# Kernel tuning notes

Hardware: AMD Instinct MI355X
Metric: run time of the kernel (lower is better)

The kernel has to match this reference:

```python
import jax, jax.numpy as jnp
import numpy as np

EPS = 1e-6
NMS_THR = 0.5
PULL_W = 1.0
PUSH_W = 1.0


def bbox_overlaps(a, b):
    # a: [M,4], b: [N,4] in (x1,y1,x2,y2) -> IoU [M,N]
    area_a = (a[:, 2] - a[:, 0]) * (a[:, 3] - a[:, 1])
    area_b = (b[:, 2] - b[:, 0]) * (b[:, 3] - b[:, 1])
    lt = jnp.maximum(a[:, None, :2], b[None, :, :2])
    rb = jnp.minimum(a[:, None, 2:], b[None, :, 2:])
    wh = jnp.clip(rb - lt, 0.0)
    inter = wh[..., 0] * wh[..., 1]
    return inter / (area_a[:, None] + area_b[None, :] - inter + EPS)


def _single_nms_loss(gti, gt_box, proposals):
    # gti: [N] int, gt_box: [G,4], proposals: [N,5]
    N = proposals.shape[0]
    G = gt_box.shape[0]
    boxes = proposals[:, :4]
    scores = proposals[:, 4]
    # push_select=True: first arg of proposal-proposal IoU is detached
    iou = bbox_overlaps(jax.lax.stop_gradient(boxes), boxes)      # [N,N]
    gpi = bbox_overlaps(gt_box, boxes)                            # [G,N]
    gpi_per = gpi[gti, jnp.arange(N)]                             # gt_proposal_iou[gt_inds[s], s]
    sg_scores = jax.lax.stop_gradient(scores)

    pos = gti >= 0
    n_pos = jnp.sum(pos)
    zero = jnp.zeros((), proposals.dtype)
    rec0 = jnp.full((G,), -1, jnp.int32)   # max_score_box_rec: gt -> box idx

    def step(carry, _):
        active, rec, pull_sum, push_sum, pull_cnt, push_cnt = carry
        any_act = jnp.any(active)
        i = jnp.argmax(jnp.where(active, scores, -jnp.inf))
        i_gt = gti[i]
        rem = active.at[i].set(False)
        has_rem = jnp.any(rem)
        body_valid = any_act & has_rem  # torch breaks before adding losses if idx empty

        # ----- pull -----
        seen = rec[i_gt] >= 0
        max_idx = jnp.maximum(rec[i_gt], 0)
        max_s_iou = jnp.maximum(iou[max_idx, i], EPS)
        pull = -jnp.log(1.0 - NMS_THR + max_s_iou) * sg_scores[i]
        pull_sum = pull_sum + jnp.where(any_act & seen & has_rem, pull, 0.0)
        pull_cnt = pull_cnt + jnp.where(any_act & seen, 1.0, 0.0)  # incremented before break
        new_val = jnp.where(any_act & ~seen, i.astype(rec.dtype), rec[i_gt])
        rec = rec.at[i_gt].set(new_val)

        # ----- push -----
        overlap = rem & (iou[i] > NMS_THR)
        push_mask = overlap & (gti != i_gt)
        has_push = jnp.any(push_mask)
        seen_s = rec[gti] >= 0  # rec already contains i_gt here (matches torch order)
        q = push_mask & (~seen_s)
        cnt = jnp.sum(q.astype(scores.dtype)) + EPS
        per = -jnp.log(EPS + gpi_per) * sg_scores
        push = jnp.sum(jnp.where(q, per, 0.0)) / cnt
        push_sum = push_sum + jnp.where(body_valid & has_push, push, 0.0)
        push_cnt = push_cnt + jnp.where(body_valid & has_push, 1.0, 0.0)

        active_next = rem & (~overlap)
        return (active_next, rec, pull_sum, push_sum, pull_cnt, push_cnt), None

    init = (pos, rec0, zero, zero, zero, zero)
    (_, _, pull_sum, push_sum, pull_cnt, push_cnt), _ = jax.lax.scan(step, init, None, length=N)

    gate = (n_pos > 1).astype(proposals.dtype)  # early-return when <=1 positive
    pull = gate * pull_sum / (pull_cnt + EPS)
    push = gate * push_sum / (push_cnt + EPS)
    return push, pull


def setup_inputs() -> dict:
    key = jax.random.key(0)
    k0, k1, k2, k3, k4, k5, k6 = jax.random.split(key, 7)
    B, N, G = 8, 2048, 64
    anchor_gt_inds = jax.random.randint(k0, (B, N), 0, G)
    # valid GT boxes: centers in a 1000x1000 image, sizes in [16,128]
    cx = jax.random.uniform(k1, (B, G)) * 1000.0
    cy = jax.random.uniform(k2, (B, G)) * 1000.0
    w = 16.0 + jax.random.uniform(k3, (B, G)) * 112.0
    h = 16.0 + jax.random.uniform(k4, (B, G)) * 112.0
    gt_bboxes = jnp.stack([cx - w / 2, cy - h / 2, cx + w / 2, cy + h / 2], axis=-1).astype(jnp.float32)
    # proposals jitter around their assigned GT so pull/push branches trigger
    pb = gt_bboxes[jnp.arange(B)[:, None], anchor_gt_inds] + jax.random.normal(k5, (B, N, 4)) * 6.0
    x1 = jnp.minimum(pb[..., 0], pb[..., 2]); x2 = jnp.maximum(pb[..., 0], pb[..., 2]) + 1.0
    y1 = jnp.minimum(pb[..., 1], pb[..., 3]); y2 = jnp.maximum(pb[..., 1], pb[..., 3]) + 1.0
    scores = jax.random.uniform(k6, (B, N))
    proposal_list = jnp.stack([x1, y1, x2, y2, scores], axis=-1).astype(jnp.float32)
    return {"gt_inds": anchor_gt_inds, "anchor_gt_inds": anchor_gt_inds,
            "gt_bboxes": gt_bboxes, "proposal_list": proposal_list}


def reference(gt_inds, anchor_gt_inds, gt_bboxes, proposal_list):
    # gt_inds is overwritten by anchor_gt_inds in the original code
    push, pull = jax.vmap(_single_nms_loss)(anchor_gt_inds, gt_bboxes, proposal_list)
    return jnp.stack([jnp.mean(push) * PUSH_W, jnp.mean(pull) * PULL_W])
```

## Files before the change

kernel.cpp:

```cpp
#include <hip/hip_runtime.h>
#include <math.h>
#include <limits.h>

#define EPSF 1e-6f
#define THR 0.5f
#define PUSH_W 1.0f
#define PULL_W 1.0f

constexpr int BN = 2048;
constexpr int BG = 64;

__device__ __forceinline__ float iou_box(float4 a, float4 b) {
  float aa = (a.z - a.x) * (a.w - a.y);
  float ab = (b.z - b.x) * (b.w - b.y);
  float w = fmaxf(fminf(a.z, b.z) - fmaxf(a.x, b.x), 0.f);
  float h = fmaxf(fminf(a.w, b.w) - fmaxf(a.y, b.y), 0.f);
  float inter = w * h;
  return inter / (aa + ab - inter + EPSF);
}

__global__ __launch_bounds__(512) void k1_sort(
    const int* __restrict__ gti_all, const float* __restrict__ gtb_all,
    const float* __restrict__ prop_all,
    float4* __restrict__ boxs, float* __restrict__ pers,
    short* __restrict__ gtss, float* __restrict__ scs,
    int* __restrict__ arrive)
{
  const int b = blockIdx.x & 7;
  const int sub = blockIdx.x >> 3;
  const int tid = threadIdx.x;
  __shared__ unsigned long long key[BN];

  if (blockIdx.x == 0 && tid == 0) *arrive = 0;

  const float* P = prop_all + (size_t)b * BN * 5;
  const int* gti = gti_all + b * BN;
  const float* GB = gtb_all + b * BG * 4;

  for (int k = 0; k < 4; ++k) {
    int j = tid + k * 512;
    key[j] = ((unsigned long long)__float_as_uint(P[j * 5 + 4]) << 32) |
             (unsigned)(BN - 1 - j);
  }
  __syncthreads();

  const int r = sub * 64 + (tid >> 3);
  const int g8 = tid & 7;
  const unsigned long long myk = key[r];
  int cnt = 0;
  const ulonglong2* K2 = (const ulonglong2*)key;
#pragma unroll 8
  for (int i = 0; i < 128; ++i) {
    ulonglong2 kk = K2[g8 + 8 * i];
    cnt += (kk.x > myk) ? 1 : 0;
    cnt += (kk.y > myk) ? 1 : 0;
  }
  cnt += __shfl_down(cnt, 4, 8);
  cnt += __shfl_down(cnt, 2, 8);
  cnt += __shfl_down(cnt, 1, 8);
  if (g8 == 0) {
    const int rank = cnt;
    int idx = (BN - 1) - (int)(myk & 0xffffffffu);
    float x1 = P[idx * 5 + 0], y1 = P[idx * 5 + 1];
    float x2 = P[idx * 5 + 2], y2 = P[idx * 5 + 3];
    float s = __uint_as_float((unsigned)(myk >> 32));
    int g = gti[idx];
    float4 bx = make_float4(x1, y1, x2, y2);
    boxs[b * BN + rank] = bx;
    scs[b * BN + rank] = s;
    gtss[b * BN + rank] = (short)g;
    float pv = 0.f;
    if (g >= 0) {
      float4 gb = make_float4(GB[g * 4], GB[g * 4 + 1], GB[g * 4 + 2], GB[g * 4 + 3]);
      pv = -logf(EPSF + iou_box(gb, bx)) * s;
    }
    pers[b * BN + rank] = pv;
  }
}

__global__ __launch_bounds__(512) void k2_adj(
    const float4* __restrict__ boxs, uint2* __restrict__ adjC)
{
  const int b  = blockIdx.x & 7;
  const int rg = (blockIdx.x >> 3) & 7;
  const int cg = blockIdx.x >> 6;
  const int tid = threadIdx.x;
  const int lane = tid & 63;
  const int w = tid >> 6;
  __shared__ float4 bs[512];

  const float4* B = boxs + b * BN;
  bs[tid] = B[cg * 512 + tid];

  const float4 r0 = B[rg * 256 +   0 + lane];
  const float4 r1 = B[rg * 256 +  64 + lane];
  const float4 r2 = B[rg * 256 + 128 + lane];
  const float4 r3 = B[rg * 256 + 192 + lane];
  const float a0 = (r0.z - r0.x) * (r0.w - r0.y) + EPSF;
  const float a1 = (r1.z - r1.x) * (r1.w - r1.y) + EPSF;
  const float a2 = (r2.z - r2.x) * (r2.w - r2.y) + EPSF;
  const float a3 = (r3.z - r3.x) * (r3.w - r3.y) + EPSF;
  __syncthreads();

  const float4* C = &bs[w * 64];
  unsigned lo0 = 0, lo1 = 0, lo2 = 0, lo3 = 0;
  unsigned hi0 = 0, hi1 = 0, hi2 = 0, hi3 = 0;

#define PRED(RR, AA, BJ, AB)                                              \
  (3.0f * (fmaxf(fminf(RR.z, BJ.z) - fmaxf(RR.x, BJ.x), 0.f) *            \
           fmaxf(fminf(RR.w, BJ.w) - fmaxf(RR.y, BJ.y), 0.f)) > AA + AB)

#pragma unroll 8
  for (int jj = 0; jj < 32; ++jj) {
    float4 bj = C[jj];
    float ab = (bj.z - bj.x) * (bj.w - bj.y);
    lo0 |= PRED(r0, a0, bj, ab) ? (1u << jj) : 0u;
    lo1 |= PRED(r1, a1, bj, ab) ? (1u << jj) : 0u;
    lo2 |= PRED(r2, a2, bj, ab) ? (1u << jj) : 0u;
    lo3 |= PRED(r3, a3, bj, ab) ? (1u << jj) : 0u;
  }
#pragma unroll 8
  for (int jj = 0; jj < 32; ++jj) {
    float4 bj = C[32 + jj];
    float ab = (bj.z - bj.x) * (bj.w - bj.y);
    hi0 |= PRED(r0, a0, bj, ab) ? (1u << jj) : 0u;
    hi1 |= PRED(r1, a1, bj, ab) ? (1u << jj) : 0u;
    hi2 |= PRED(r2, a2, bj, ab) ? (1u << jj) : 0u;
    hi3 |= PRED(r3, a3, bj, ab) ? (1u << jj) : 0u;
  }
#undef PRED

  const int c = cg * 8 + w;
  uint2* CO = adjC + ((size_t)b * 32 + c) * 2048;
  CO[rg * 256 +   0 + lane] = make_uint2(lo0, hi0);
  CO[rg * 256 +  64 + lane] = make_uint2(lo1, hi1);
  CO[rg * 256 + 128 + lane] = make_uint2(lo2, hi2);
  CO[rg * 256 + 192 + lane] = make_uint2(lo3, hi3);
}

#define QR(B, K, Q) B##_##K##_##Q

#define DECL16(B) \
  uint2 QR(B,0,0), QR(B,0,1), QR(B,0,2), QR(B,0,3), \
        QR(B,1,0), QR(B,1,1), QR(B,1,2), QR(B,1,3), \
        QR(B,2,0), QR(B,2,1), QR(B,2,2), QR(B,2,3), \
        QR(B,3,0), QR(B,3,1), QR(B,3,2), QR(B,3,3);

#define LOADCH(B, K, C) \
  QR(B,K,0) = Cb[(size_t)(C) * 2048 + wbase]; \
  QR(B,K,1) = Cb[(size_t)(C) * 2048 + wbase + 64]; \
  QR(B,K,2) = Cb[(size_t)(C) * 2048 + wbase + 128]; \
  QR(B,K,3) = Cb[(size_t)(C) * 2048 + wbase + 192];

#define LOAD16(B, RR) \
  LOADCH(B, 0, (RR)*4+0) LOADCH(B, 1, (RR)*4+1) \
  LOADCH(B, 2, (RR)*4+2) LOADCH(B, 3, (RR)*4+3)

#define PICK(B, K, C)                                                          \
  {                                                                            \
    unsigned mybit = ((act >> (K)) & ~(supG >> (K))) & 1u;                     \
    unsigned long long row64 =                                                 \
        ((unsigned long long)QR(B,K,K).y << 32) |                              \
        (unsigned long long)QR(B,K,K).x;                                       \
    unsigned long long pickw = 0ull;                                           \
    unsigned long long bal = __ballot(mybit != 0u);                            \
    while (bal) {                                                              \
      int bpos = (int)__ffsll(bal) - 1;                                        \
      pickw |= 1ull << bpos;                                                   \
      mybit &= ~(unsigned)((row64 >> bpos) & 1ull);                            \
      bal = __ballot(mybit != 0u);                                             \
    }                                                                          \
    if (lane == 0) {                                                           \
      pm_lds[2 * (C)] = (unsigned)pickw;                                       \
      pm_lds[2 * (C) + 1] = (unsigned)(pickw >> 32);                           \
    }                                                                          \
    if (pickw != 0ull) {                                                       \
      unsigned pwlo = (unsigned)pickw, pwhi = (unsigned)(pickw >> 32);         \
      { unsigned hit = (QR(B,K,0).x & pwlo) | (QR(B,K,0).y & pwhi); supG |= (hit ? 1u : 0u); }      \
      { unsigned hit = (QR(B,K,1).x & pwlo) | (QR(B,K,1).y & pwhi); supG |= (hit ? 2u : 0u); }      \
      { unsigned hit = (QR(B,K,2).x & pwlo) | (QR(B,K,2).y & pwhi); supG |= (hit ? 4u : 0u); }      \
      { unsigned hit = (QR(B,K,3).x & pwlo) | (QR(B,K,3).y & pwhi); supG |= (hit ? 8u : 0u); }      \
    }                                                                          \
  }

#define APPLY(B, K, C)                                                         \
  {                                                                            \
    unsigned pwlo = pm_lds[2 * (C)], pwhi = pm_lds[2 * (C) + 1];               \
    if ((pwlo | pwhi) != 0u) {                                                 \
      unsigned nbits = 0;                                                      \
      { unsigned hit = (QR(B,K,0).x & pwlo) | (QR(B,K,0).y & pwhi); nbits |= hit ? 1u : 0u; }       \
      { unsigned hit = (QR(B,K,1).x & pwlo) | (QR(B,K,1).y & pwhi); nbits |= hit ? 2u : 0u; }       \
      { unsigned hit = (QR(B,K,2).x & pwlo) | (QR(B,K,2).y & pwhi); nbits |= hit ? 4u : 0u; }       \
      { unsigned hit = (QR(B,K,3).x & pwlo) | (QR(B,K,3).y & pwhi); nbits |= hit ? 8u : 0u; }       \
      unsigned flips = nbits & ~sup;                                           \
      sup |= nbits;                                                            \
      while (flips) {                                                          \
        int fq = __ffs(flips) - 1; flips &= flips - 1;                         \
        fsc_s[wbase + fq * 64] = (unsigned char)(C);                           \
      }                                                                        \
    }                                                                          \
  }

#define ROUND(RR, CUR, NXT)                                                    \
  {                                                                            \
    if ((RR) + 1 < 8) { LOAD16(NXT, (RR) + 1) }                                \
    if (wave == (RR)) {                                                        \
      unsigned supG = sup;                                                     \
      PICK(CUR, 0, (RR)*4 + 0)                                                 \
      PICK(CUR, 1, (RR)*4 + 1)                                                 \
      PICK(CUR, 2, (RR)*4 + 2)                                                 \
      PICK(CUR, 3, (RR)*4 + 3)                                                 \
      asm volatile("s_waitcnt lgkmcnt(0)" ::: "memory");                       \
    }                                                                          \
    __builtin_amdgcn_s_barrier();                                              \
    asm volatile("" ::: "memory");                                             \
    APPLY(CUR, 0, (RR)*4 + 0)                                                  \
    APPLY(CUR, 1, (RR)*4 + 1)                                                  \
    APPLY(CUR, 2, (RR)*4 + 2)                                                  \
    APPLY(CUR, 3, (RR)*4 + 3)                                                  \
  }

__global__ __launch_bounds__(512, 1) void k3_fused(
    const float4* __restrict__ boxs, const float* __restrict__ pers,
    const short* __restrict__ gtss, const float* __restrict__ scs,
    const uint2* __restrict__ adjC, float* __restrict__ bp,
    int* __restrict__ arrive, float* __restrict__ out, int nb)
{
  const int b = blockIdx.x;
  const int tid = threadIdx.x;
  const int lane = tid & 63;
  const int wave = tid >> 6;

  __shared__ float qs_s[BN];
  __shared__ int qc_s[BN];
  __shared__ unsigned short ev_s[BN];
  __shared__ short gts_s[BN];
  __shared__ unsigned char fsc_s[BN];
  __shared__ unsigned pm_lds[64];
  __shared__ unsigned pre_s[64];
  __shared__ int fpr_s[64];
  __shared__ unsigned hp_s[64];
  __shared__ int lastrem_s, npick_s, npos_s;
  __shared__ float redp[8][4];

  const uint2* Cb = adjC + (size_t)b * 32 * 2048;
  const int wbase = wave * 256 + lane;

  for (int k = tid; k < BN / 2; k += 512)
    ((int*)gts_s)[k] = ((const int*)(gtss + b * BN))[k];
  for (int k = tid; k < BN; k += 512) { qs_s[k] = 0.f; qc_s[k] = 0; }
  for (int k = tid; k < BN; k += 512) fsc_s[k] = 255;
  if (tid < 64) { fpr_s[tid] = INT_MAX; hp_s[tid] = 0u; }
  if (tid == 0) { lastrem_s = 0; npos_s = 0; }
  __syncthreads();

  DECL16(X)
  DECL16(Y)
  LOAD16(X, 0)

  unsigned act = 0;
  if (gts_s[wbase +   0] >= 0) act |= 1u;
  if (gts_s[wbase +  64] >= 0) act |= 2u;
  if (gts_s[wbase + 128] >= 0) act |= 4u;
  if (gts_s[wbase + 192] >= 0) act |= 8u;
  {
    int cnt = __popc(act);
    for (int o = 1; o < 64; o <<= 1) cnt += __shfl_xor(cnt, o);
    if (lane == 0) atomicAdd(&npos_s, cnt);
  }
  unsigned sup = 0;

  ROUND(0, X, Y) ROUND(1, Y, X) ROUND(2, X, Y) ROUND(3, Y, X)
  ROUND(4, X, Y) ROUND(5, Y, X) ROUND(6, X, Y) ROUND(7, Y, X)

  __syncthreads();

  if (tid < 64) {
    int s = 0;
    for (int w = 0; w < tid; ++w) s += __popc(pm_lds[w]);
    pre_s[tid] = (unsigned)s;
  }
  __syncthreads();
  if (tid == 0) npick_s = (int)pre_s[63] + __popc(pm_lds[63]);
  if (wave == 0) {
    unsigned wbits = pm_lds[lane];
    int e = (int)pre_s[lane];
    while (wbits) {
      int bpos = __ffs(wbits) - 1; wbits &= wbits - 1;
      int rank = lane * 32 + bpos;
      ev_s[e] = (unsigned short)rank;
      atomicMin(&fpr_s[(int)gts_s[rank]], rank);
      e++;
    }
  }
  __syncthreads();

  const int P = npick_s;
  {
    const int j0 = tid, j1 = tid + 512, j2 = tid + 1024, j3 = tid + 1536;
    const int c0 = fsc_s[j0], c1 = fsc_s[j1], c2 = fsc_s[j2], c3 = fsc_s[j3];
    uint2 v0 = make_uint2(0, 0), v1 = v0, v2 = v0, v3 = v0;
    if (c0 != 255) v0 = Cb[(size_t)c0 * 2048 + j0];
    if (c1 != 255) v1 = Cb[(size_t)c1 * 2048 + j1];
    if (c2 != 255) v2 = Cb[(size_t)c2 * 2048 + j2];
    if (c3 != 255) v3 = Cb[(size_t)c3 * 2048 + j3];

#define PROCD(J, C, V)                                                         \
  {                                                                            \
    int gj = (int)gts_s[J];                                                    \
    if ((C) != 255 && gj >= 0) {                                               \
      unsigned m0 = V.x & pm_lds[2 * (C)];                                     \
      unsigned m1 = V.y & pm_lds[2 * (C) + 1];                                 \
      int frank = m0 ? ((C) * 64 + __ffs(m0) - 1)                              \
                     : ((C) * 64 + 32 + __ffs(m1) - 1);                        \
      if (frank != (J)) {                                                      \
        int e = (int)pre_s[frank >> 5] +                                       \
                __popc(pm_lds[frank >> 5] & ((1u << (frank & 31)) - 1u));      \
        if (e == P - 1) lastrem_s = 1;                                         \
        int gt = (int)gts_s[frank];                                            \
        if (gj != gt) {                                                        \
          atomicOr(&hp_s[e >> 5], 1u << (e & 31));                             \
          if (fpr_s[gj] > frank) {                                             \
            atomicAdd(&qs_s[e], pers[b * BN + (J)]);                           \
            atomicAdd(&qc_s[e], 1);                                            \
          }                                                                    \
        }                                                                      \
      }                                                                        \
    }                                                                          \
  }

    PROCD(j0, c0, v0)
    PROCD(j1, c1, v1)
    PROCD(j2, c2, v2)
    PROCD(j3, c3, v3)
#undef PROCD
  }
  __syncthreads();

  const int lastrem = lastrem_s;
  const int npos = npos_s;
  float pull_l = 0.f, pcl = 0.f, push_l = 0.f, pshl = 0.f;
  for (int t = tid; t < P; t += 512) {
    int r = (int)ev_s[t];
    int g = (int)gts_s[r];
    int fp = fpr_s[g];
    bool seen = (fp < r);
    bool hr = (t < P - 1) || (lastrem != 0);
    if (seen) {
      pcl += 1.f;
      if (hr) {
        float4 bA = boxs[b * BN + fp];
        float4 bB = boxs[b * BN + r];
        float io = iou_box(bA, bB);
        pull_l += -logf(1.f - THR + fmaxf(io, EPSF)) * scs[b * BN + r];
      }
    }
    if (hr && ((hp_s[t >> 5] >> (t & 31)) & 1u)) {
      pshl += 1.f;
      push_l += qs_s[t] / ((float)qc_s[t] + EPSF);
    }
  }
  for (int o = 1; o < 64; o <<= 1) {
    pull_l += __shfl_xor(pull_l, o);
    pcl    += __shfl_xor(pcl, o);
    push_l += __shfl_xor(push_l, o);
    pshl   += __shfl_xor(pshl, o);
  }
  if (lane == 0) { redp[wave][0] = pull_l; redp[wave][1] = pcl; redp[wave][2] = push_l; redp[wave][3] = pshl; }
  __syncthreads();
  if (tid == 0) {
    float Ps = 0.f, Pc = 0.f, Ss = 0.f, Sc = 0.f;
    for (int w = 0; w < 8; ++w) { Ps += redp[w][0]; Pc += redp[w][1]; Ss += redp[w][2]; Sc += redp[w][3]; }
    float gate = (npos > 1) ? 1.f : 0.f;
    bp[b * 2 + 0] = gate * Ss / (Sc + EPSF);
    bp[b * 2 + 1] = gate * Ps / (Pc + EPSF);
    __threadfence();
    int old = atomicAdd(arrive, 1);
    if (old == nb - 1) {
      __threadfence();
      float ps = 0.f, pl = 0.f;
      for (int i = 0; i < nb; ++i) { ps += bp[2 * i]; pl += bp[2 * i + 1]; }
      float inv = 1.f / (float)nb;
      out[0] = ps * inv * PUSH_W;
      out[1] = pl * inv * PULL_W;
      *arrive = 0;
    }
  }
}

constexpr int NT = 256;
constexpr int PT = BN / NT;
constexpr int NW = NT / 64;

__global__ void nms_finalize_kernel(const float* __restrict__ bp, float* __restrict__ out, int nb) {
  if (threadIdx.x == 0 && blockIdx.x == 0) {
    float ps = 0.f, pl = 0.f;
    for (int b = 0; b < nb; ++b) { ps += bp[2 * b]; pl += bp[2 * b + 1]; }
    float inv = 1.f / (float)nb;
    out[0] = ps * inv * PUSH_W;
    out[1] = pl * inv * PULL_W;
  }
}

__global__ __launch_bounds__(NT) void nms_loss_kernel(
    const int* __restrict__ gti_all, const float* __restrict__ gtb_all,
    const float* __restrict__ prop_all, float* __restrict__ out_bp)
{
  const int b = blockIdx.x;
  const int tid = threadIdx.x;
  const int lane = tid & 63;
  const int wave = tid >> 6;

  __shared__ float4 box[BN];
  __shared__ float sc[BN];
  __shared__ float per[BN];
  __shared__ int gts[BN];
  __shared__ unsigned char act[BN];
  __shared__ int rec[BG];
  __shared__ float rs[NW];
  __shared__ int ri[NW];
  __shared__ int rrem[NW];
  __shared__ int rqc[NW];
  __shared__ float rqs[NW];
  __shared__ int rany[NW];
  __shared__ int sh_nact;
  __shared__ int sh_ig;
  __shared__ float4 sh_ibox;

  const int* gti = gti_all + b * BN;
  const float* GB = gtb_all + b * BG * 4;
  const float* P = prop_all + (size_t)b * BN * 5;

  int local_pos = 0;
  for (int k = 0; k < PT; ++k) {
    int j = tid + k * NT;
    float x1 = P[j * 5 + 0], y1 = P[j * 5 + 1];
    float x2 = P[j * 5 + 2], y2 = P[j * 5 + 3];
    float s = P[j * 5 + 4];
    box[j] = make_float4(x1, y1, x2, y2);
    sc[j] = s;
    int g = gti[j];
    gts[j] = g;
    unsigned char a = (g >= 0) ? 1 : 0;
    act[j] = a;
    local_pos += a;
    float pv = 0.f;
    if (g >= 0) {
      float4 gb = make_float4(GB[g * 4], GB[g * 4 + 1], GB[g * 4 + 2], GB[g * 4 + 3]);
      float i2 = iou_box(gb, make_float4(x1, y1, x2, y2));
      pv = -logf(EPSF + i2) * s;
    }
    per[j] = pv;
  }
  if (tid < BG) rec[tid] = -1;
  for (int off = 32; off; off >>= 1) local_pos += __shfl_down(local_pos, off);
  if (lane == 0) rrem[wave] = local_pos;
  __syncthreads();
  int n_pos = 0;
  if (tid == 0) {
    for (int w = 0; w < NW; ++w) n_pos += rrem[w];
    sh_nact = n_pos;
  }
  float pull_sum = 0.f, push_sum = 0.f, pull_cnt = 0.f, push_cnt = 0.f;
  int t0_hasrem = 0;
  __syncthreads();

  while (true) {
    int nact = sh_nact;
    if (nact <= 0) break;
    float bs = -INFINITY;
    int bi = BN;
    for (int k = 0; k < PT; ++k) {
      int j = tid + k * NT;
      if (act[j]) {
        float s = sc[j];
        if (s > bs || (s == bs && j < bi)) { bs = s; bi = j; }
      }
    }
    for (int off = 32; off; off >>= 1) {
      float os = __shfl_down(bs, off);
      int oi = __shfl_down(bi, off);
      if (os > bs || (os == bs && oi < bi)) { bs = os; bi = oi; }
    }
    if (lane == 0) { rs[wave] = bs; ri[wave] = bi; }
    __syncthreads();
    if (tid == 0) {
      float cs = rs[0]; int ci = ri[0];
      for (int w = 1; w < NW; ++w)
        if (rs[w] > cs || (rs[w] == cs && ri[w] < ci)) { cs = rs[w]; ci = ri[w]; }
      int i = ci;
      int ig = gts[i];
      act[i] = 0;
      t0_hasrem = (nact - 1 > 0);
      int r = rec[ig];
      if (r >= 0) {
        pull_cnt += 1.f;
        if (t0_hasrem) {
          float i2 = iou_box(box[r], box[i]);
          float m = fmaxf(i2, EPSF);
          pull_sum += -logf(1.f - THR + m) * sc[i];
        }
      } else {
        rec[ig] = i;
      }
      sh_ig = ig; sh_ibox = box[i];
    }
    __syncthreads();
    float4 ib = sh_ibox;
    int igx = sh_ig;
    int removed = 0, qcc = 0, anyp = 0;
    float qss = 0.f;
    for (int k = 0; k < PT; ++k) {
      int j = tid + k * NT;
      if (act[j]) {
        float i2 = iou_box(ib, box[j]);
        if (i2 > THR) {
          act[j] = 0;
          removed++;
          int gj = gts[j];
          if (gj != igx) {
            anyp = 1;
            if (rec[gj] < 0) { qcc++; qss += per[j]; }
          }
        }
      }
    }
    for (int off = 32; off; off >>= 1) {
      removed += __shfl_down(removed, off);
      qcc += __shfl_down(qcc, off);
      qss += __shfl_down(qss, off);
      anyp |= __shfl_down(anyp, off);
    }
    if (lane == 0) { rrem[wave] = removed; rqc[wave] = qcc; rqs[wave] = qss; rany[wave] = anyp; }
    __syncthreads();
    if (tid == 0) {
      int rm = 0, qct = 0, ap = 0; float qst = 0.f;
      for (int w = 0; w < NW; ++w) { rm += rrem[w]; qct += rqc[w]; qst += rqs[w]; ap |= rany[w]; }
      sh_nact = nact - 1 - rm;
      if (t0_hasrem && ap) {
        push_sum += qst / ((float)qct + EPSF);
        push_cnt += 1.f;
      }
    }
    __syncthreads();
  }

  if (tid == 0) {
    float gate = (n_pos > 1) ? 1.f : 0.f;
    out_bp[b * 2 + 0] = gate * push_sum / (push_cnt + EPSF);
    out_bp[b * 2 + 1] = gate * pull_sum / (pull_cnt + EPSF);
  }
}

extern "C" void kernel_launch(void* const* d_in, const int* in_sizes, int n_in,
                              void* d_out, int out_size, void* d_ws, size_t ws_size,
                              hipStream_t stream) {
  const int* gti = (const int*)d_in[1];
  const float* gtb = (const float*)d_in[2];
  const float* props = (const float*)d_in[3];
  float* out = (float*)d_out;
  const int nb = in_sizes[1] / BN;

  const size_t off_adj  = 0;
  const size_t off_box  = off_adj  + (size_t)nb * BN * 64 * 4;
  const size_t off_per  = off_box  + (size_t)nb * BN * 16;
  const size_t off_sc   = off_per  + (size_t)nb * BN * 4;
  const size_t off_gts  = off_sc   + (size_t)nb * BN * 4;
  const size_t off_bp   = off_gts  + (size_t)nb * BN * 2;
  const size_t off_arr  = off_bp   + (size_t)nb * 2 * 4;
  const size_t needed   = off_arr + 64;

  if (ws_size >= needed && nb == 8) {
    char* ws = (char*)d_ws;
    uint2* adjC = (uint2*)(ws + off_adj);
    float4* boxs = (float4*)(ws + off_box);
    float* pers = (float*)(ws + off_per);
    float* scs = (float*)(ws + off_sc);
    short* gtss = (short*)(ws + off_gts);
    float* bp = (float*)(ws + off_bp);
    int* arrive = (int*)(ws + off_arr);

    k1_sort<<<nb * 32, 512, 0, stream>>>(gti, gtb, props, boxs, pers, gtss, scs, arrive);
    k2_adj<<<nb * 32, 512, 0, stream>>>(boxs, adjC);
    k3_fused<<<nb, 512, 0, stream>>>(boxs, pers, gtss, scs, adjC, bp, arrive, out, nb);
  } else {
    float* bp = (float*)d_ws;
    nms_loss_kernel<<<nb, NT, 0, stream>>>(gti, gtb, props, bp);
    nms_finalize_kernel<<<1, 64, 0, stream>>>(bp, out, nb);
  }
}
```

Measured before the change: 53.74 us.

## Fuse sort, adjacency and NMS kernels into one persistent kernel with grid barriers

Merges the three kernels (rank sort, IoU adjacency bitmask, fused NMS loss) into a single 256-block kernel. Software grid barriers built on agent-scope atomics replace the kernel boundaries, and a small init kernel resets the barrier counters. Shared memory is reused through one arena across phases. This removes inter-kernel launch gaps, but it depends on all 256 blocks being co-resident for the spinning barrier to make progress, and only 8 blocks do the serial NMS phase while the rest exit.

Measured after the change: 92.35 us. +71.8%, slower.

```diff
diff --git a/kernel.cpp b/kernel.cpp
--- a/kernel.cpp
+++ b/kernel.cpp
@@ -19,123 +19,28 @@
   return inter / (aa + ab - inter + EPSF);
 }
 
-__global__ __launch_bounds__(512) void k1_sort(
-    const int* __restrict__ gti_all, const float* __restrict__ gtb_all,
-    const float* __restrict__ prop_all,
-    float4* __restrict__ boxs, float* __restrict__ pers,
-    short* __restrict__ gtss, float* __restrict__ scs,
-    int* __restrict__ arrive)
-{
-  const int b = blockIdx.x & 7;
-  const int sub = blockIdx.x >> 3;
-  const int tid = threadIdx.x;
-  __shared__ unsigned long long key[BN];
-
-  if (blockIdx.x == 0 && tid == 0) *arrive = 0;
-
-  const float* P = prop_all + (size_t)b * BN * 5;
-  const int* gti = gti_all + b * BN;
-  const float* GB = gtb_all + b * BG * 4;
-
-  for (int k = 0; k < 4; ++k) {
-    int j = tid + k * 512;
-    key[j] = ((unsigned long long)__float_as_uint(P[j * 5 + 4]) << 32) |
-             (unsigned)(BN - 1 - j);
-  }
+__global__ void init_kernel(int* __restrict__ bar) {
+  if (threadIdx.x == 0) { bar[0] = 0; bar[1] = 0; bar[2] = 0; bar[3] = 0; }
+}
+
+__device__ __forceinline__ void gridbar(int* bar, int slot, int target_gen,
+                                        int nblk, bool spin) {
   __syncthreads();
-
-  const int r = sub * 64 + (tid >> 3);
-  const int g8 = tid & 7;
-  const unsigned long long myk = key[r];
-  int cnt = 0;
-  const ulonglong2* K2 = (const ulonglong2*)key;
-#pragma unroll 8
-  for (int i = 0; i < 128; ++i) {
-    ulonglong2 kk = K2[g8 + 8 * i];
-    cnt += (kk.x > myk) ? 1 : 0;
-    cnt += (kk.y > myk) ? 1 : 0;
-  }
-  cnt += __shfl_down(cnt, 4, 8);
-  cnt += __shfl_down(cnt, 2, 8);
-  cnt += __shfl_down(cnt, 1, 8);
-  if (g8 == 0) {
-    const int rank = cnt;
-    int idx = (BN - 1) - (int)(myk & 0xffffffffu);
-    float x1 = P[idx * 5 + 0], y1 = P[idx * 5 + 1];
-    float x2 = P[idx * 5 + 2], y2 = P[idx * 5 + 3];
-    float s = __uint_as_float((unsigned)(myk >> 32));
-    int g = gti[idx];
-    float4 bx = make_float4(x1, y1, x2, y2);
-    boxs[b * BN + rank] = bx;
-    scs[b * BN + rank] = s;
-    gtss[b * BN + rank] = (short)g;
-    float pv = 0.f;
-    if (g >= 0) {
-      float4 gb = make_float4(GB[g * 4], GB[g * 4 + 1], GB[g * 4 + 2], GB[g * 4 + 3]);
-      pv = -logf(EPSF + iou_box(gb, bx)) * s;
-    }
-    pers[b * BN + rank] = pv;
-  }
-}
-
-__global__ __launch_bounds__(512) void k2_adj(
-    const float4* __restrict__ boxs, uint2* __restrict__ adjC)
-{
-  const int b  = blockIdx.x & 7;
-  const int rg = (blockIdx.x >> 3) & 7;
-  const int cg = blockIdx.x >> 6;
-  const int tid = threadIdx.x;
-  const int lane = tid & 63;
-  const int w = tid >> 6;
-  __shared__ float4 bs[512];
-
-  const float4* B = boxs + b * BN;
-  bs[tid] = B[cg * 512 + tid];
-
-  const float4 r0 = B[rg * 256 +   0 + lane];
-  const float4 r1 = B[rg * 256 +  64 + lane];
-  const float4 r2 = B[rg * 256 + 128 + lane];
-  const float4 r3 = B[rg * 256 + 192 + lane];
-  const float a0 = (r0.z - r0.x) * (r0.w - r0.y) + EPSF;
-  const float a1 = (r1.z - r1.x) * (r1.w - r1.y) + EPSF;
-  const float a2 = (r2.z - r2.x) * (r2.w - r2.y) + EPSF;
-  const float a3 = (r3.z - r3.x) * (r3.w - r3.y) + EPSF;
+  if (threadIdx.x == 0) {
+    __threadfence();
+    int prev = __hip_atomic_fetch_add(&bar[slot], 1, __ATOMIC_ACQ_REL,
+                                      __HIP_MEMORY_SCOPE_AGENT);
+    if (prev == nblk - 1) {
+      __hip_atomic_fetch_add(&bar[2], 1, __ATOMIC_ACQ_REL,
+                             __HIP_MEMORY_SCOPE_AGENT);
+    } else if (spin) {
+      while (__hip_atomic_load(&bar[2], __ATOMIC_ACQUIRE,
+                               __HIP_MEMORY_SCOPE_AGENT) < target_gen)
+        __builtin_amdgcn_s_sleep(8);
+    }
+    __threadfence();
+  }
   __syncthreads();
-
-  const float4* C = &bs[w * 64];
-  unsigned lo0 = 0, lo1 = 0, lo2 = 0, lo3 = 0;
-  unsigned hi0 = 0, hi1 = 0, hi2 = 0, hi3 = 0;
-
-#define PRED(RR, AA, BJ, AB)                                              \
-  (3.0f * (fmaxf(fminf(RR.z, BJ.z) - fmaxf(RR.x, BJ.x), 0.f) *            \
-           fmaxf(fminf(RR.w, BJ.w) - fmaxf(RR.y, BJ.y), 0.f)) > AA + AB)
-
-#pragma unroll 8
-  for (int jj = 0; jj < 32; ++jj) {
-    float4 bj = C[jj];
-    float ab = (bj.z - bj.x) * (bj.w - bj.y);
-    lo0 |= PRED(r0, a0, bj, ab) ? (1u << jj) : 0u;
-    lo1 |= PRED(r1, a1, bj, ab) ? (1u << jj) : 0u;
-    lo2 |= PRED(r2, a2, bj, ab) ? (1u << jj) : 0u;
-    lo3 |= PRED(r3, a3, bj, ab) ? (1u << jj) : 0u;
-  }
-#pragma unroll 8
-  for (int jj = 0; jj < 32; ++jj) {
-    float4 bj = C[32 + jj];
-    float ab = (bj.z - bj.x) * (bj.w - bj.y);
-    hi0 |= PRED(r0, a0, bj, ab) ? (1u << jj) : 0u;
-    hi1 |= PRED(r1, a1, bj, ab) ? (1u << jj) : 0u;
-    hi2 |= PRED(r2, a2, bj, ab) ? (1u << jj) : 0u;
-    hi3 |= PRED(r3, a3, bj, ab) ? (1u << jj) : 0u;
-  }
-#undef PRED
-
-  const int c = cg * 8 + w;
-  uint2* CO = adjC + ((size_t)b * 32 + c) * 2048;
-  CO[rg * 256 +   0 + lane] = make_uint2(lo0, hi0);
-  CO[rg * 256 +  64 + lane] = make_uint2(lo1, hi1);
-  CO[rg * 256 + 128 + lane] = make_uint2(lo2, hi2);
-  CO[rg * 256 + 192 + lane] = make_uint2(lo3, hi3);
 }
 
 #define QR(B, K, Q) B##_##K##_##Q
@@ -220,22 +125,21 @@
     APPLY(CUR, 3, (RR)*4 + 3)                                                  \
   }
 
-__global__ __launch_bounds__(512, 1) void k3_fused(
-    const float4* __restrict__ boxs, const float* __restrict__ pers,
-    const short* __restrict__ gtss, const float* __restrict__ scs,
-    const uint2* __restrict__ adjC, float* __restrict__ bp,
-    int* __restrict__ arrive, float* __restrict__ out, int nb)
+__global__ __launch_bounds__(512, 1) void mega2(
+    const int* __restrict__ gti_all, const float* __restrict__ gtb_all,
+    const float* __restrict__ prop_all,
+    float4* __restrict__ boxs, float* __restrict__ pers,
+    short* __restrict__ gtss, float* __restrict__ scs,
+    uint2* __restrict__ adjC, float* __restrict__ bp,
+    int* __restrict__ bar, float* __restrict__ out, int nb)
 {
-  const int b = blockIdx.x;
+  const int blk = blockIdx.x;
   const int tid = threadIdx.x;
   const int lane = tid & 63;
   const int wave = tid >> 6;
-
-  __shared__ float qs_s[BN];
-  __shared__ int qc_s[BN];
-  __shared__ unsigned short ev_s[BN];
-  __shared__ short gts_s[BN];
-  __shared__ unsigned char fsc_s[BN];
+  const int b8 = blk & 7;
+
+  __shared__ __align__(16) unsigned char arena[26624];
   __shared__ unsigned pm_lds[64];
   __shared__ unsigned pre_s[64];
   __shared__ int fpr_s[64];
@@ -243,67 +147,180 @@
   __shared__ int lastrem_s, npick_s, npos_s;
   __shared__ float redp[8][4];
 
-  const uint2* Cb = adjC + (size_t)b * 32 * 2048;
-  const int wbase = wave * 256 + lane;
-
-  for (int k = tid; k < BN / 2; k += 512)
-    ((int*)gts_s)[k] = ((const int*)(gtss + b * BN))[k];
-  for (int k = tid; k < BN; k += 512) { qs_s[k] = 0.f; qc_s[k] = 0; }
-  for (int k = tid; k < BN; k += 512) fsc_s[k] = 255;
-  if (tid < 64) { fpr_s[tid] = INT_MAX; hp_s[tid] = 0u; }
-  if (tid == 0) { lastrem_s = 0; npos_s = 0; }
-  __syncthreads();
-
-  DECL16(X)
-  DECL16(Y)
-  LOAD16(X, 0)
-
-  unsigned act = 0;
-  if (gts_s[wbase +   0] >= 0) act |= 1u;
-  if (gts_s[wbase +  64] >= 0) act |= 2u;
-  if (gts_s[wbase + 128] >= 0) act |= 4u;
-  if (gts_s[wbase + 192] >= 0) act |= 8u;
   {
-    int cnt = __popc(act);
-    for (int o = 1; o < 64; o <<= 1) cnt += __shfl_xor(cnt, o);
-    if (lane == 0) atomicAdd(&npos_s, cnt);
-  }
-  unsigned sup = 0;
-
-  ROUND(0, X, Y) ROUND(1, Y, X) ROUND(2, X, Y) ROUND(3, Y, X)
-  ROUND(4, X, Y) ROUND(5, Y, X) ROUND(6, X, Y) ROUND(7, Y, X)
-
-  __syncthreads();
-
-  if (tid < 64) {
-    int s = 0;
-    for (int w = 0; w < tid; ++w) s += __popc(pm_lds[w]);
-    pre_s[tid] = (unsigned)s;
-  }
-  __syncthreads();
-  if (tid == 0) npick_s = (int)pre_s[63] + __popc(pm_lds[63]);
-  if (wave == 0) {
-    unsigned wbits = pm_lds[lane];
-    int e = (int)pre_s[lane];
-    while (wbits) {
-      int bpos = __ffs(wbits) - 1; wbits &= wbits - 1;
-      int rank = lane * 32 + bpos;
-      ev_s[e] = (unsigned short)rank;
-      atomicMin(&fpr_s[(int)gts_s[rank]], rank);
-      e++;
-    }
-  }
-  __syncthreads();
-
-  const int P = npick_s;
+    unsigned long long* key = (unsigned long long*)arena;
+    const int sub = blk >> 3;
+    const float* P = prop_all + (size_t)b8 * BN * 5;
+    const int* gti = gti_all + b8 * BN;
+    const float* GB = gtb_all + b8 * BG * 4;
+
+    for (int k = 0; k < 4; ++k) {
+      int j = tid + k * 512;
+      key[j] = ((unsigned long long)__float_as_uint(P[j * 5 + 4]) << 32) |
+               (unsigned)(BN - 1 - j);
+    }
+    __syncthreads();
+
+    const int r = sub * 64 + (tid >> 3);
+    const int g8 = tid & 7;
+    const unsigned long long myk = key[r];
+    int cnt = 0;
+    const ulonglong2* K2 = (const ulonglong2*)key;
+#pragma unroll 8
+    for (int i = 0; i < 128; ++i) {
+      ulonglong2 kk = K2[g8 + 8 * i];
+      cnt += (kk.x > myk) ? 1 : 0;
+      cnt += (kk.y > myk) ? 1 : 0;
+    }
+    cnt += __shfl_down(cnt, 4, 8);
+    cnt += __shfl_down(cnt, 2, 8);
+    cnt += __shfl_down(cnt, 1, 8);
+    if (g8 == 0) {
+      const int rank = cnt;
+      int idx = (BN - 1) - (int)(myk & 0xffffffffu);
+      float x1 = P[idx * 5 + 0], y1 = P[idx * 5 + 1];
+      float x2 = P[idx * 5 + 2], y2 = P[idx * 5 + 3];
+      float s = __uint_as_float((unsigned)(myk >> 32));
+      int g = gti[idx];
+      float4 bx = make_float4(x1, y1, x2, y2);
+      boxs[b8 * BN + rank] = bx;
+      scs[b8 * BN + rank] = s;
+      gtss[b8 * BN + rank] = (short)g;
+      float pv = 0.f;
+      if (g >= 0) {
+        float4 gb = make_float4(GB[g * 4], GB[g * 4 + 1], GB[g * 4 + 2], GB[g * 4 + 3]);
+        pv = -logf(EPSF + iou_box(gb, bx)) * s;
+      }
+      pers[b8 * BN + rank] = pv;
+    }
+  }
+  gridbar(bar, 0, 1, 256, true);
+
   {
-    const int j0 = tid, j1 = tid + 512, j2 = tid + 1024, j3 = tid + 1536;
-    const int c0 = fsc_s[j0], c1 = fsc_s[j1], c2 = fsc_s[j2], c3 = fsc_s[j3];
-    uint2 v0 = make_uint2(0, 0), v1 = v0, v2 = v0, v3 = v0;
-    if (c0 != 255) v0 = Cb[(size_t)c0 * 2048 + j0];
-    if (c1 != 255) v1 = Cb[(size_t)c1 * 2048 + j1];
-    if (c2 != 255) v2 = Cb[(size_t)c2 * 2048 + j2];
-    if (c3 != 255) v3 = Cb[(size_t)c3 * 2048 + j3];
+    float4* bs = (float4*)arena;
+    const int rg = (blk >> 3) & 7;
+    const int cg = blk >> 6;
+    const int w = wave;
+    const float4* B = boxs + b8 * BN;
+    bs[tid] = B[cg * 512 + tid];
+
+    const float4 r0 = B[rg * 256 +   0 + lane];
+    const float4 r1 = B[rg * 256 +  64 + lane];
+    const float4 r2 = B[rg * 256 + 128 + lane];
+    const float4 r3 = B[rg * 256 + 192 + lane];
+    const float a0 = (r0.z - r0.x) * (r0.w - r0.y) + EPSF;
+    const float a1 = (r1.z - r1.x) * (r1.w - r1.y) + EPSF;
+    const float a2 = (r2.z - r2.x) * (r2.w - r2.y) + EPSF;
+    const float a3 = (r3.z - r3.x) * (r3.w - r3.y) + EPSF;
+    __syncthreads();
+
+    const float4* C = &bs[w * 64];
+    unsigned lo0 = 0, lo1 = 0, lo2 = 0, lo3 = 0;
+    unsigned hi0 = 0, hi1 = 0, hi2 = 0, hi3 = 0;
+
+#define PRED(RR, AA, BJ, AB)                                              \
+  (3.0f * (fmaxf(fminf(RR.z, BJ.z) - fmaxf(RR.x, BJ.x), 0.f) *            \
+           fmaxf(fminf(RR.w, BJ.w) - fmaxf(RR.y, BJ.y), 0.f)) > AA + AB)
+
+#pragma unroll 8
+    for (int jj = 0; jj < 32; ++jj) {
+      float4 bj = C[jj];
+      float ab = (bj.z - bj.x) * (bj.w - bj.y);
+      lo0 |= PRED(r0, a0, bj, ab) ? (1u << jj) : 0u;
+      lo1 |= PRED(r1, a1, bj, ab) ? (1u << jj) : 0u;
+      lo2 |= PRED(r2, a2, bj, ab) ? (1u << jj) : 0u;
+      lo3 |= PRED(r3, a3, bj, ab) ? (1u << jj) : 0u;
+    }
+#pragma unroll 8
+    for (int jj = 0; jj < 32; ++jj) {
+      float4 bj = C[32 + jj];
+      float ab = (bj.z - bj.x) * (bj.w - bj.y);
+      hi0 |= PRED(r0, a0, bj, ab) ? (1u << jj) : 0u;
+      hi1 |= PRED(r1, a1, bj, ab) ? (1u << jj) : 0u;
+      hi2 |= PRED(r2, a2, bj, ab) ? (1u << jj) : 0u;
+      hi3 |= PRED(r3, a3, bj, ab) ? (1u << jj) : 0u;
+    }
+#undef PRED
+
+    const int c = cg * 8 + w;
+    uint2* CO = adjC + ((size_t)b8 * 32 + c) * 2048;
+    CO[rg * 256 +   0 + lane] = make_uint2(lo0, hi0);
+    CO[rg * 256 +  64 + lane] = make_uint2(lo1, hi1);
+    CO[rg * 256 + 128 + lane] = make_uint2(lo2, hi2);
+    CO[rg * 256 + 192 + lane] = make_uint2(lo3, hi3);
+  }
+  gridbar(bar, 1, 2, 256, blk < nb);
+  if (blk >= nb) return;
+
+  {
+    const int b = blk;
+    float* qs_s = (float*)arena;
+    int* qc_s = (int*)(arena + 8192);
+    unsigned short* ev_s = (unsigned short*)(arena + 16384);
+    short* gts_s = (short*)(arena + 20480);
+    unsigned char* fsc_s = arena + 24576;
+
+    const uint2* Cb = adjC + (size_t)b * 32 * 2048;
+    const int wbase = wave * 256 + lane;
+
+    for (int k = tid; k < BN / 2; k += 512)
+      ((int*)gts_s)[k] = ((const int*)(gtss + b * BN))[k];
+    for (int k = tid; k < BN; k += 512) { qs_s[k] = 0.f; qc_s[k] = 0; }
+    for (int k = tid; k < BN; k += 512) fsc_s[k] = 255;
+    if (tid < 64) { fpr_s[tid] = INT_MAX; hp_s[tid] = 0u; }
+    if (tid == 0) { lastrem_s = 0; npos_s = 0; }
+    __syncthreads();
+
+    DECL16(X)
+    DECL16(Y)
+    LOAD16(X, 0)
+
+    unsigned act = 0;
+    if (gts_s[wbase +   0] >= 0) act |= 1u;
+    if (gts_s[wbase +  64] >= 0) act |= 2u;
+    if (gts_s[wbase + 128] >= 0) act |= 4u;
+    if (gts_s[wbase + 192] >= 0) act |= 8u;
+    {
+      int cnt = __popc(act);
+      for (int o = 1; o < 64; o <<= 1) cnt += __shfl_xor(cnt, o);
+      if (lane == 0) atomicAdd(&npos_s, cnt);
+    }
+    unsigned sup = 0;
+
+    ROUND(0, X, Y) ROUND(1, Y, X) ROUND(2, X, Y) ROUND(3, Y, X)
+    ROUND(4, X, Y) ROUND(5, Y, X) ROUND(6, X, Y) ROUND(7, Y, X)
+
+    __syncthreads();
+
+    if (tid < 64) {
+      int s = 0;
+      for (int w = 0; w < tid; ++w) s += __popc(pm_lds[w]);
+      pre_s[tid] = (unsigned)s;
+    }
+    __syncthreads();
+    if (tid == 0) npick_s = (int)pre_s[63] + __popc(pm_lds[63]);
+    if (wave == 0) {
+      unsigned wbits = pm_lds[lane];
+      int e = (int)pre_s[lane];
+      while (wbits) {
+        int bpos = __ffs(wbits) - 1; wbits &= wbits - 1;
+        int rank = lane * 32 + bpos;
+        ev_s[e] = (unsigned short)rank;
+        atomicMin(&fpr_s[(int)gts_s[rank]], rank);
+        e++;
+      }
+    }
+    __syncthreads();
+
+    const int P = npick_s;
+    {
+      const int j0 = tid, j1 = tid + 512, j2 = tid + 1024, j3 = tid + 1536;
+      const int c0 = fsc_s[j0], c1 = fsc_s[j1], c2 = fsc_s[j2], c3 = fsc_s[j3];
+      uint2 v0 = make_uint2(0, 0), v1 = v0, v2 = v0, v3 = v0;
+      if (c0 != 255) v0 = Cb[(size_t)c0 * 2048 + j0];
+      if (c1 != 255) v1 = Cb[(size_t)c1 * 2048 + j1];
+      if (c2 != 255) v2 = Cb[(size_t)c2 * 2048 + j2];
+      if (c3 != 255) v3 = Cb[(size_t)c3 * 2048 + j3];
 
 #define PROCD(J, C, V)                                                         \
   {                                                                            \
@@ -329,61 +346,61 @@
     }                                                                          \
   }
 
-    PROCD(j0, c0, v0)
-    PROCD(j1, c1, v1)
-    PROCD(j2, c2, v2)
-    PROCD(j3, c3, v3)
+      PROCD(j0, c0, v0)
+      PROCD(j1, c1, v1)
+      PROCD(j2, c2, v2)
+      PROCD(j3, c3, v3)
 #undef PROCD
-  }
-  __syncthreads();
-
-  const int lastrem = lastrem_s;
-  const int npos = npos_s;
-  float pull_l = 0.f, pcl = 0.f, push_l = 0.f, pshl = 0.f;
-  for (int t = tid; t < P; t += 512) {
-    int r = (int)ev_s[t];
-    int g = (int)gts_s[r];
-    int fp = fpr_s[g];
-    bool seen = (fp < r);
-    bool hr = (t < P - 1) || (lastrem != 0);
-    if (seen) {
-      pcl += 1.f;
-      if (hr) {
-        float4 bA = boxs[b * BN + fp];
-        float4 bB = boxs[b * BN + r];
-        float io = iou_box(bA, bB);
-        pull_l += -logf(1.f - THR + fmaxf(io, EPSF)) * scs[b * BN + r];
-      }
-    }
-    if (hr && ((hp_s[t >> 5] >> (t & 31)) & 1u)) {
-      pshl += 1.f;
-      push_l += qs_s[t] / ((float)qc_s[t] + EPSF);
-    }
-  }
-  for (int o = 1; o < 64; o <<= 1) {
-    pull_l += __shfl_xor(pull_l, o);
-    pcl    += __shfl_xor(pcl, o);
-    push_l += __shfl_xor(push_l, o);
-    pshl   += __shfl_xor(pshl, o);
-  }
-  if (lane == 0) { redp[wave][0] = pull_l; redp[wave][1] = pcl; redp[wave][2] = push_l; redp[wave][3] = pshl; }
-  __syncthreads();
-  if (tid == 0) {
-    float Ps = 0.f, Pc = 0.f, Ss = 0.f, Sc = 0.f;
-    for (int w = 0; w < 8; ++w) { Ps += redp[w][0]; Pc += redp[w][1]; Ss += redp[w][2]; Sc += redp[w][3]; }
-    float gate = (npos > 1) ? 1.f : 0.f;
-    bp[b * 2 + 0] = gate * Ss / (Sc + EPSF);
-    bp[b * 2 + 1] = gate * Ps / (Pc + EPSF);
-    __threadfence();
-    int old = atomicAdd(arrive, 1);
-    if (old == nb - 1) {
+    }
+    __syncthreads();
+
+    const int lastrem = lastrem_s;
+    const int npos = npos_s;
+    float pull_l = 0.f, pcl = 0.f, push_l = 0.f, pshl = 0.f;
+    for (int t = tid; t < P; t += 512) {
+      int r = (int)ev_s[t];
+      int g = (int)gts_s[r];
+      int fp = fpr_s[g];
+      bool seen = (fp < r);
+      bool hr = (t < P - 1) || (lastrem != 0);
+      if (seen) {
+        pcl += 1.f;
+        if (hr) {
+          float4 bA = boxs[b * BN + fp];
+          float4 bB = boxs[b * BN + r];
+          float io = iou_box(bA, bB);
+          pull_l += -logf(1.f - THR + fmaxf(io, EPSF)) * scs[b * BN + r];
+        }
+      }
+      if (hr && ((hp_s[t >> 5] >> (t & 31)) & 1u)) {
+        pshl += 1.f;
+        push_l += qs_s[t] / ((float)qc_s[t] + EPSF);
+      }
+    }
+    for (int o = 1; o < 64; o <<= 1) {
+      pull_l += __shfl_xor(pull_l, o);
+      pcl    += __shfl_xor(pcl, o);
+      push_l += __shfl_xor(push_l, o);
+      pshl   += __shfl_xor(pshl, o);
+    }
+    if (lane == 0) { redp[wave][0] = pull_l; redp[wave][1] = pcl; redp[wave][2] = push_l; redp[wave][3] = pshl; }
+    __syncthreads();
+    if (tid == 0) {
+      float Ps = 0.f, Pc = 0.f, Ss = 0.f, Sc = 0.f;
+      for (int w = 0; w < 8; ++w) { Ps += redp[w][0]; Pc += redp[w][1]; Ss += redp[w][2]; Sc += redp[w][3]; }
+      float gate = (npos > 1) ? 1.f : 0.f;
+      bp[b * 2 + 0] = gate * Ss / (Sc + EPSF);
+      bp[b * 2 + 1] = gate * Ps / (Pc + EPSF);
       __threadfence();
-      float ps = 0.f, pl = 0.f;
-      for (int i = 0; i < nb; ++i) { ps += bp[2 * i]; pl += bp[2 * i + 1]; }
-      float inv = 1.f / (float)nb;
-      out[0] = ps * inv * PUSH_W;
-      out[1] = pl * inv * PULL_W;
-      *arrive = 0;
+      int old = atomicAdd(&bar[3], 1);
+      if (old == nb - 1) {
+        __threadfence();
+        float ps = 0.f, pl = 0.f;
+        for (int i = 0; i < nb; ++i) { ps += bp[2 * i]; pl += bp[2 * i + 1]; }
+        float inv = 1.f / (float)nb;
+        out[0] = ps * inv * PUSH_W;
+        out[1] = pl * inv * PULL_W;
+      }
     }
   }
 }
@@ -567,8 +584,8 @@
   const size_t off_sc   = off_per  + (size_t)nb * BN * 4;
   const size_t off_gts  = off_sc   + (size_t)nb * BN * 4;
   const size_t off_bp   = off_gts  + (size_t)nb * BN * 2;
-  const size_t off_arr  = off_bp   + (size_t)nb * 2 * 4;
-  const size_t needed   = off_arr + 64;
+  const size_t off_bar  = off_bp   + (size_t)nb * 2 * 4;
+  const size_t needed   = off_bar + 64;
 
   if (ws_size >= needed && nb == 8) {
     char* ws = (char*)d_ws;
@@ -578,11 +595,11 @@
     float* scs = (float*)(ws + off_sc);
     short* gtss = (short*)(ws + off_gts);
     float* bp = (float*)(ws + off_bp);
-    int* arrive = (int*)(ws + off_arr);
-
-    k1_sort<<<nb * 32, 512, 0, stream>>>(gti, gtb, props, boxs, pers, gtss, scs, arrive);
-    k2_adj<<<nb * 32, 512, 0, stream>>>(boxs, adjC);
-    k3_fused<<<nb, 512, 0, stream>>>(boxs, pers, gtss, scs, adjC, bp, arrive, out, nb);
+    int* bar = (int*)(ws + off_bar);
+
+    init_kernel<<<1, 64, 0, stream>>>(bar);
+    mega2<<<256, 512, 0, stream>>>(gti, gtb, props, boxs, pers, gtss, scs,
+                                   adjC, bp, bar, out, nb);
   } else {
     float* bp = (float*)d_ws;
     nms_loss_kernel<<<nb, NT, 0, stream>>>(gti, gtb, props, bp);
```
